# Kernel optimization log

Hardware: AMD Instinct MI355X
Metric: run time of the kernel (lower is better)

Reference implementation:

```python
import jax, jax.numpy as jnp
import numpy as np

N = 100000          # num_nodes
E = 1250000         # num_edges
H = 64              # node_hidden_size
T = 2               # num_rounds


def setup_inputs() -> dict:
    key = jax.random.key(0)
    ks = jax.random.split(key, 10)
    s = 0.1  # init scale for weights
    return {
        "x": jax.random.normal(ks[0], (N, H), dtype=jnp.float32),
        "edge_index": jax.random.randint(ks[1], (2, E), 0, N, dtype=jnp.int64),
        "edge_attr": jax.random.normal(ks[2], (E, 1), dtype=jnp.float32),
        # message layers: Linear(2H+1 -> H), one per round
        "msg_W": jax.random.normal(ks[3], (T, H, 2 * H + 1), dtype=jnp.float32) * s,
        "msg_b": jax.random.normal(ks[4], (T, H), dtype=jnp.float32) * s,
        # GRUCell params, gate order (r, z, n) as in torch
        "gru_Wih": jax.random.normal(ks[5], (T, 3 * H, H), dtype=jnp.float32) * s,
        "gru_bih": jax.random.normal(ks[6], (T, 3 * H), dtype=jnp.float32) * s,
        "gru_Whh": jax.random.normal(ks[7], (T, 3 * H, H), dtype=jnp.float32) * s,
        "gru_bhh": jax.random.normal(ks[8], (T, 3 * H), dtype=jnp.float32) * s,
    }


def _gru_cell(inp, h, Wih, bih, Whh, bhh):
    # torch.nn.GRUCell math, gate order r, z, n
    gi = inp @ Wih.T + bih   # [N, 3H]
    gh = h @ Whh.T + bhh     # [N, 3H]
    i_r, i_z, i_n = jnp.split(gi, 3, axis=1)
    h_r, h_z, h_n = jnp.split(gh, 3, axis=1)
    r = jax.nn.sigmoid(i_r + h_r)
    z = jax.nn.sigmoid(i_z + h_z)
    n = jnp.tanh(i_n + r * h_n)
    return (1.0 - z) * n + z * h


def reference(x, edge_index, edge_attr, msg_W, msg_b, gru_Wih, gru_bih, gru_Whh, gru_bhh):
    row, col = edge_index[0], edge_index[1]
    num_rounds = msg_W.shape[0]
    for t in range(num_rounds):
        src = x[row]    # [E, H]
        dest = x[col]   # [E, H]
        m_input = jnp.concatenate([dest, src, edge_attr], axis=1)  # [E, 2H+1]
        messages = m_input @ msg_W[t].T + msg_b[t]                 # [E, H]
        agg = jax.ops.segment_sum(messages, row, num_segments=x.shape[0])  # [N, H]
        x = _gru_cell(agg, x, gru_Wih[t], gru_bih[t], gru_Whh[t], gru_bhh[t])
    return x
```

## Files before the change

kernel.cpp:

```cpp
#include <hip/hip_runtime.h>
#include <hip/hip_bf16.h>
#include <hip/hip_fp16.h>

#define H 64
#define CAP 48

typedef __attribute__((ext_vector_type(8))) short short8;
typedef __attribute__((ext_vector_type(4))) float float4v;

__device__ __forceinline__ short f2bf_bits(float f) {
    union { __hip_bfloat16 b; short s; } u;
    u.b = __float2bfloat16(f);
    return u.s;
}
__device__ __forceinline__ float bf2f(unsigned short s) {
    union { unsigned int u; float f; } v;
    v.u = ((unsigned int)s) << 16;
    return v.f;
}
__device__ __forceinline__ void split8(const float* p, short8& hi, short8& lo) {
    float4v f0 = *(const float4v*)p;
    float4v f1 = *(const float4v*)(p + 4);
#pragma unroll
    for (int j = 0; j < 8; j++) {
        float f = (j < 4) ? f0[j] : f1[j - 4];
        short h = f2bf_bits(f);
        float fh = bf2f((unsigned short)h);
        hi[j] = h;
        lo[j] = f2bf_bits(f - fh);
    }
}
__device__ __forceinline__ void zero8(short8& hi, short8& lo) {
#pragma unroll
    for (int j = 0; j < 8; j++) { hi[j] = 0; lo[j] = 0; }
}

#define MFMA(a, b, c) __builtin_amdgcn_mfma_f32_16x16x32_bf16(a, b, c, 0, 0, 0)

__global__ __launch_bounds__(256) void count_prep(
    const int* __restrict__ row, int* __restrict__ deg, int* __restrict__ lpos,
    int E, int EB,
    const float* __restrict__ msg_W,
    const float* __restrict__ Wih, const float* __restrict__ Whh,
    short* __restrict__ msgfrag, short* __restrict__ grufrag, int T)
{
    if ((int)blockIdx.x < EB) {
        int e = blockIdx.x * 256 + threadIdx.x;
        if (e < E) lpos[e] = atomicAdd(&deg[row[e]], 1);
        return;
    }
    const int lane = threadIdx.x & 63;
    int unit = (blockIdx.x - EB) * 4 + (threadIdx.x >> 6);
    const int kq = (lane >> 4) * 8;
    if (unit < T * 16) {
        const int slot = unit & 15, t = unit >> 4;
        const int tile = slot >> 1, ks = slot & 1;
        const float* W = msg_W + (size_t)t * H * 129;
        const int wrow = (tile & 3) * 16 + (lane & 15);
        const int coff = (tile < 4) ? 0 : 64;
        short8 hi, lo;
        split8(W + (size_t)wrow * 129 + coff + ks * 32 + kq, hi, lo);
        short8* out = (short8*)(msgfrag + (size_t)t * 16384);
        out[slot * 64 + lane] = hi;
        out[16 * 64 + slot * 64 + lane] = lo;
    } else {
        unit -= T * 16;
        if (unit >= T * 48) return;
        const int slot = unit % 48, t = unit / 48;
        const int tile = slot >> 1, ks = slot & 1;
        const float* Wp = (tile < 12)
            ? (Wih + (size_t)t * 192 * H + ((size_t)(tile * 16 + (lane & 15))) * H)
            : (Whh + (size_t)t * 192 * H + ((size_t)((tile - 12) * 16 + (lane & 15))) * H);
        short8 hi, lo;
        split8(Wp + ks * 32 + kq, hi, lo);
        short8* out = (short8*)(grufrag + (size_t)t * 49152);
        out[slot * 64 + lane] = hi;
        out[48 * 64 + slot * 64 + lane] = lo;
    }
}

__global__ __launch_bounds__(256) void scatter_cast(
    const int* __restrict__ row, const int* __restrict__ col,
    const float* __restrict__ attr, const int* __restrict__ lpos,
    int2* __restrict__ edata, int E, int EB,
    const float* __restrict__ x_in, __half* __restrict__ xh, int NH8)
{
    if ((int)blockIdx.x < EB) {
        int e = blockIdx.x * 256 + threadIdx.x;
        if (e < E) {
            int p = lpos[e];
            if (p < CAP) {
                int2 v;
                v.x = col[e];
                v.y = __float_as_int(attr[e]);
                edata[(size_t)row[e] * CAP + p] = v;
            }
        }
    } else {
        int i = (blockIdx.x - EB) * 256 + threadIdx.x;
        if (i < NH8) {
            const float* p = x_in + (size_t)i * 8;
            float4v f0 = *(const float4v*)p;
            float4v f1 = *(const float4v*)(p + 4);
            short8 hv;
#pragma unroll
            for (int u = 0; u < 8; u++) {
                float f = (u < 4) ? f0[u] : f1[u - 4];
                hv[u] = __half_as_short(__float2half(f));
            }
            *(short8*)(xh + (size_t)i * 8) = hv;
        }
    }
}

__global__ __launch_bounds__(256) void aggregate(
    const int* __restrict__ deg, const int2* __restrict__ edata,
    const __half* __restrict__ xh,
    short* __restrict__ s_hi, short* __restrict__ s_lo,
    float2* __restrict__ asum2, int N)
{
    const int tid = threadIdx.x, lane = tid & 63, wv = tid >> 6;
    const int g = lane >> 3, cl = lane & 7;
    const int n = (blockIdx.x * 4 + wv) * 8 + g;
    int cnt = 0;
    if (n < N) { cnt = deg[n]; if (cnt > CAP) cnt = CAP; }
    const int2* ebase = edata + (size_t)n * CAP;
    float acc[8] = {0.f,0.f,0.f,0.f,0.f,0.f,0.f,0.f};
    float aacc = 0.f;
    for (int j = 0; j < cnt; j += 8) {
        int2 e[8];
#pragma unroll
        for (int u = 0; u < 8; u++) {
            int idx = j + u; if (idx > cnt - 1) idx = cnt - 1;
            e[u] = ebase[idx];
        }
        short8 h[8];
#pragma unroll
        for (int u = 0; u < 8; u++) {
            int c = e[u].x;
            c = (c < 0) ? 0 : (c >= N ? N - 1 : c);
            h[u] = *(const short8*)(xh + (size_t)c * H + cl * 8);
        }
#pragma unroll
        for (int u = 0; u < 8; u++) {
            const bool val = (j + u < cnt);
            const float w = val ? 1.f : 0.f;
            aacc += val ? __int_as_float(e[u].y) : 0.f;
#pragma unroll
            for (int k = 0; k < 8; k++)
                acc[k] = fmaf(w, __half2float(__ushort_as_half((unsigned short)h[u][k])), acc[k]);
        }
    }
    if (n < N) {
        short8 hi8, lo8;
#pragma unroll
        for (int u = 0; u < 8; u++) {
            float v = acc[u];
            short hbits = f2bf_bits(v);
            hi8[u] = hbits;
            lo8[u] = f2bf_bits(v - bf2f((unsigned short)hbits));
        }
        *(short8*)(s_hi + (size_t)n * H + cl * 8) = hi8;
        *(short8*)(s_lo + (size_t)n * H + cl * 8) = lo8;
        if (cl == 0) asum2[n] = make_float2(aacc, (float)cnt);
    }
}

#define SLD 68
__global__ __launch_bounds__(256) void fused_msg_gru(
    const short* __restrict__ s_hi, const short* __restrict__ s_lo,
    const float2* __restrict__ asum2,
    const float* xf,
    float* x, __half* __restrict__ xh,
    const short* __restrict__ mfrag, const short* __restrict__ gfrag,
    const float* __restrict__ Wt, const float* __restrict__ mb,
    const float* __restrict__ bih, const float* __restrict__ bhh,
    int N, int write_xh)
{
    __shared__ float scratch[4][16 * SLD];
    const int tid = threadIdx.x, lane = tid & 63, wv = tid >> 6;
    const int base = blockIdx.x * 64 + wv * 16;
    if (base >= N) return;
    const int arow = lane & 15;
    const int kq = (lane >> 4) * 8;
    const int colb = lane & 15;
    const int rq4 = (lane >> 4) * 4;
    const int m_a = base + arow;
    const bool mv = (m_a < N);
    const short8* mhi = (const short8*)mfrag;
    const short8* mlo = mhi + 16 * 64;
    const short8* ghi = (const short8*)gfrag;
    const short8* glo = ghi + 48 * 64;
    float* scr = scratch[wv];

    short8 sfh[2], sfl[2], xfh[2], xfl[2];
#pragma unroll
    for (int ks = 0; ks < 2; ks++) {
        if (mv) {
            sfh[ks] = *(const short8*)(s_hi + (size_t)m_a * H + ks * 32 + kq);
            sfl[ks] = *(const short8*)(s_lo + (size_t)m_a * H + ks * 32 + kq);
            split8(xf + (size_t)m_a * H + ks * 32 + kq, xfh[ks], xfl[ks]);
        } else { zero8(sfh[ks], sfl[ks]); zero8(xfh[ks], xfl[ks]); }
    }
    float2 da[4];
#pragma unroll
    for (int r = 0; r < 4; r++) {
        const int m = base + rq4 + r;
        da[r] = (m < N) ? asum2[m] : make_float2(0.f, 0.f);
    }

    float4v accd[4], accs[4];
#pragma unroll
    for (int ct = 0; ct < 4; ct++) {
        accd[ct] = (float4v){0.f, 0.f, 0.f, 0.f};
        accs[ct] = (float4v){0.f, 0.f, 0.f, 0.f};
    }
#pragma unroll
    for (int ks = 0; ks < 2; ks++) {
#pragma unroll
        for (int ct = 0; ct < 4; ct++) {
            short8 bh = mhi[(ct * 2 + ks) * 64 + lane];
            short8 bl = mlo[(ct * 2 + ks) * 64 + lane];
            accd[ct] = MFMA(sfh[ks], bh, accd[ct]);
            accd[ct] = MFMA(sfl[ks], bh, accd[ct]);
            accd[ct] = MFMA(sfh[ks], bl, accd[ct]);
            short8 ch = mhi[((4 + ct) * 2 + ks) * 64 + lane];
            short8 cl8 = mlo[((4 + ct) * 2 + ks) * 64 + lane];
            accs[ct] = MFMA(xfh[ks], ch, accs[ct]);
            accs[ct] = MFMA(xfl[ks], ch, accs[ct]);
            accs[ct] = MFMA(xfh[ks], cl8, accs[ct]);
        }
    }

#pragma unroll
    for (int ct = 0; ct < 4; ct++) {
        const int j = ct * 16 + colb;
        const float bj = mb[j];
        const float wa = Wt[(size_t)j * 129 + 128];
#pragma unroll
        for (int r = 0; r < 4; r++) {
            float v = accd[ct][r] + da[r].y * (accs[ct][r] + bj) + da[r].x * wa;
            scr[(rq4 + r) * SLD + j] = v;
        }
    }
    asm volatile("s_waitcnt lgkmcnt(0)" ::: "memory");
    short8 agh[2], agl[2];
#pragma unroll
    for (int ks = 0; ks < 2; ks++)
        split8(scr + arow * SLD + ks * 32 + kq, agh[ks], agl[ks]);

#pragma unroll
    for (int ct = 0; ct < 4; ct++) {
        float4v ai[3], ao[3];
#pragma unroll
        for (int g2 = 0; g2 < 3; g2++) {
            ai[g2] = (float4v){0.f, 0.f, 0.f, 0.f};
            ao[g2] = (float4v){0.f, 0.f, 0.f, 0.f};
        }
#pragma unroll
        for (int ks = 0; ks < 2; ks++) {
#pragma unroll
            for (int g2 = 0; g2 < 3; g2++) {
                short8 bh = ghi[((g2 * 4 + ct) * 2 + ks) * 64 + lane];
                short8 bl = glo[((g2 * 4 + ct) * 2 + ks) * 64 + lane];
                ai[g2] = MFMA(agh[ks], bh, ai[g2]);
                ai[g2] = MFMA(agl[ks], bh, ai[g2]);
                ai[g2] = MFMA(agh[ks], bl, ai[g2]);
                short8 hh = ghi[((12 + g2 * 4 + ct) * 2 + ks) * 64 + lane];
                short8 hl = glo[((12 + g2 * 4 + ct) * 2 + ks) * 64 + lane];
                ao[g2] = MFMA(xfh[ks], hh, ao[g2]);
                ao[g2] = MFMA(xfl[ks], hh, ao[g2]);
                ao[g2] = MFMA(xfh[ks], hl, ao[g2]);
            }
        }
        const int j = ct * 16 + colb;
        const float b_ir = bih[j], b_iz = bih[64 + j], b_in = bih[128 + j];
        const float b_hr = bhh[j], b_hz = bhh[64 + j], b_hn = bhh[128 + j];
#pragma unroll
        for (int r = 0; r < 4; r++) {
            const int m = base + rq4 + r;
            float ir = ai[0][r] + b_ir;
            float iz = ai[1][r] + b_iz;
            float in_ = ai[2][r] + b_in;
            float hr = ao[0][r] + b_hr;
            float hz = ao[1][r] + b_hz;
            float hn = ao[2][r] + b_hn;
            float rr = 1.f / (1.f + __expf(-(ir + hr)));
            float zz = 1.f / (1.f + __expf(-(iz + hz)));
            float e2 = __expf(2.f * (in_ + rr * hn));
            float nn = 1.f - 2.f / (e2 + 1.f);
            float hold = (m < N) ? xf[(size_t)m * H + j] : 0.f;
            scr[(rq4 + r) * SLD + j] = (1.f - zz) * nn + zz * hold;
        }
    }
    asm volatile("s_waitcnt lgkmcnt(0)" ::: "memory");

    if (mv) {
        float4v o[4];
#pragma unroll
        for (int q4 = 0; q4 < 4; q4++)
            o[q4] = *(const float4v*)(scr + arow * SLD + (lane >> 4) * 16 + q4 * 4);
        float4v* xp = (float4v*)(x + (size_t)m_a * H + (lane >> 4) * 16);
        xp[0] = o[0]; xp[1] = o[1]; xp[2] = o[2]; xp[3] = o[3];
        if (write_xh) {
            short8 hv0, hv1;
#pragma unroll
            for (int u = 0; u < 8; u++) {
                hv0[u] = __half_as_short(__float2half(o[u >> 2][u & 3]));
                hv1[u] = __half_as_short(__float2half(o[2 + (u >> 2)][u & 3]));
            }
            *(short8*)(xh + (size_t)m_a * H + (lane >> 4) * 16) = hv0;
            *(short8*)(xh + (size_t)m_a * H + (lane >> 4) * 16 + 8) = hv1;
        }
    }
}

extern "C" void kernel_launch(void* const* d_in, const int* in_sizes, int n_in,
                              void* d_out, int out_size, void* d_ws, size_t ws_size,
                              hipStream_t stream) {
    const float* x_in  = (const float*)d_in[0];
    const int*   ei    = (const int*)d_in[1];
    const float* attr  = (const float*)d_in[2];
    const float* msg_W = (const float*)d_in[3];
    const float* msg_b = (const float*)d_in[4];
    const float* Wih   = (const float*)d_in[5];
    const float* bih   = (const float*)d_in[6];
    const float* Whh   = (const float*)d_in[7];
    const float* bhh   = (const float*)d_in[8];

    const int N = in_sizes[0] / H;
    const int E = in_sizes[2];
    const int T = in_sizes[4] / H;
    const int* row = ei;
    const int* col = ei + E;

    float*  x       = (float*)d_out;
    short*  s_hi    = (short*)d_ws;
    short*  s_lo    = s_hi + (size_t)N * H;
    int*    lpos    = (int*)s_lo;
    __half* xh      = (__half*)(s_lo + (size_t)N * H);
    float2* asum2   = (float2*)(xh + (size_t)N * H);
    int*    deg     = (int*)(asum2 + N);
    int2*   edata   = (int2*)(deg + N);
    short*  msgfrag = (short*)(edata + (size_t)N * CAP);
    short*  grufrag = msgfrag + (size_t)T * 16384;

    const int eb  = (E + 255) / 256;
    const int nh8 = (N * H) / 8;
    const int cb  = (nh8 + 255) / 256;
    const int pb  = (T * 16 + T * 48 + 3) / 4;

    hipMemsetAsync(deg, 0, (size_t)N * sizeof(int), stream);

    count_prep<<<eb + pb, 256, 0, stream>>>(
        row, deg, lpos, E, eb, msg_W, Wih, Whh, msgfrag, grufrag, T);
    scatter_cast<<<eb + cb, 256, 0, stream>>>(
        row, col, attr, lpos, edata, E, eb, x_in, xh, nh8);

    const int nbq        = (N + 63) / 64;
    const int agg_blocks = (N + 31) / 32;

    for (int t = 0; t < T; t++) {
        aggregate<<<agg_blocks, 256, 0, stream>>>(
            deg, edata, xh, s_hi, s_lo, asum2, N);
        fused_msg_gru<<<nbq, 256, 0, stream>>>(
            s_hi, s_lo, asum2,
            (t == 0) ? x_in : x, x, xh,
            msgfrag + (size_t)t * 16384, grufrag + (size_t)t * 49152,
            msg_W + (size_t)t * H * (2 * H + 1), msg_b + (size_t)t * H,
            bih + (size_t)t * 3 * H, bhh + (size_t)t * 3 * H,
            N, (t + 1 < T) ? 1 : 0);
    }
}
```

Measured before the change: 343.6 us.

## Split edge counting across kernels, widen aggregate unroll, stage GRU weights in LDS

Edge counting is split into two halves: the first half's degree counting runs alongside weight prep and the fp16 cast of x, and the second half's counting runs alongside the scatter of the first half. This is meant to overlap atomic counting with scatter writes instead of running them in strict sequence. The aggregate kernel moves to 64-thread blocks and gathers 16 neighbours per iteration instead of 8, giving more loads in flight per wave. The fused GRU kernel now copies its 96KB of weight fragments into shared memory before computing, which costs LDS capacity and may reduce occupancy.

```diff
diff --git a/kernel.cpp b/kernel.cpp
--- a/kernel.cpp
+++ b/kernel.cpp
@@ -37,57 +37,79 @@
 
 #define MFMA(a, b, c) __builtin_amdgcn_mfma_f32_16x16x32_bf16(a, b, c, 0, 0, 0)
 
-__global__ __launch_bounds__(256) void count_prep(
+__global__ __launch_bounds__(256) void count_a(
     const int* __restrict__ row, int* __restrict__ deg, int* __restrict__ lpos,
-    int E, int EB,
+    int e1, int EB, int PB,
     const float* __restrict__ msg_W,
     const float* __restrict__ Wih, const float* __restrict__ Whh,
-    short* __restrict__ msgfrag, short* __restrict__ grufrag, int T)
-{
-    if ((int)blockIdx.x < EB) {
-        int e = blockIdx.x * 256 + threadIdx.x;
-        if (e < E) lpos[e] = atomicAdd(&deg[row[e]], 1);
-        return;
-    }
-    const int lane = threadIdx.x & 63;
-    int unit = (blockIdx.x - EB) * 4 + (threadIdx.x >> 6);
-    const int kq = (lane >> 4) * 8;
-    if (unit < T * 16) {
-        const int slot = unit & 15, t = unit >> 4;
-        const int tile = slot >> 1, ks = slot & 1;
-        const float* W = msg_W + (size_t)t * H * 129;
-        const int wrow = (tile & 3) * 16 + (lane & 15);
-        const int coff = (tile < 4) ? 0 : 64;
-        short8 hi, lo;
-        split8(W + (size_t)wrow * 129 + coff + ks * 32 + kq, hi, lo);
-        short8* out = (short8*)(msgfrag + (size_t)t * 16384);
-        out[slot * 64 + lane] = hi;
-        out[16 * 64 + slot * 64 + lane] = lo;
-    } else {
-        unit -= T * 16;
-        if (unit >= T * 48) return;
-        const int slot = unit % 48, t = unit / 48;
-        const int tile = slot >> 1, ks = slot & 1;
-        const float* Wp = (tile < 12)
-            ? (Wih + (size_t)t * 192 * H + ((size_t)(tile * 16 + (lane & 15))) * H)
-            : (Whh + (size_t)t * 192 * H + ((size_t)((tile - 12) * 16 + (lane & 15))) * H);
-        short8 hi, lo;
-        split8(Wp + ks * 32 + kq, hi, lo);
-        short8* out = (short8*)(grufrag + (size_t)t * 49152);
-        out[slot * 64 + lane] = hi;
-        out[48 * 64 + slot * 64 + lane] = lo;
-    }
-}
-
-__global__ __launch_bounds__(256) void scatter_cast(
-    const int* __restrict__ row, const int* __restrict__ col,
-    const float* __restrict__ attr, const int* __restrict__ lpos,
-    int2* __restrict__ edata, int E, int EB,
+    short* __restrict__ msgfrag, short* __restrict__ grufrag, int T,
     const float* __restrict__ x_in, __half* __restrict__ xh, int NH8)
 {
     if ((int)blockIdx.x < EB) {
         int e = blockIdx.x * 256 + threadIdx.x;
-        if (e < E) {
+        if (e < e1) lpos[e] = atomicAdd(&deg[row[e]], 1);
+        return;
+    }
+    int u = blockIdx.x - EB;
+    if (u < PB) {
+        const int lane = threadIdx.x & 63;
+        int unit = u * 4 + (threadIdx.x >> 6);
+        const int kq = (lane >> 4) * 8;
+        if (unit < T * 16) {
+            const int slot = unit & 15, t = unit >> 4;
+            const int tile = slot >> 1, ks = slot & 1;
+            const float* W = msg_W + (size_t)t * H * 129;
+            const int wrow = (tile & 3) * 16 + (lane & 15);
+            const int coff = (tile < 4) ? 0 : 64;
+            short8 hi, lo;
+            split8(W + (size_t)wrow * 129 + coff + ks * 32 + kq, hi, lo);
+            short8* out = (short8*)(msgfrag + (size_t)t * 16384);
+            out[slot * 64 + lane] = hi;
+            out[16 * 64 + slot * 64 + lane] = lo;
+        } else {
+            unit -= T * 16;
+            if (unit >= T * 48) return;
+            const int slot = unit % 48, t = unit / 48;
+            const int tile = slot >> 1, ks = slot & 1;
+            const float* Wp = (tile < 12)
+                ? (Wih + (size_t)t * 192 * H + ((size_t)(tile * 16 + (lane & 15))) * H)
+                : (Whh + (size_t)t * 192 * H + ((size_t)((tile - 12) * 16 + (lane & 15))) * H);
+            short8 hi, lo;
+            split8(Wp + ks * 32 + kq, hi, lo);
+            short8* out = (short8*)(grufrag + (size_t)t * 49152);
+            out[slot * 64 + lane] = hi;
+            out[48 * 64 + slot * 64 + lane] = lo;
+        }
+    } else {
+        int i = (u - PB) * 256 + threadIdx.x;
+        if (i < NH8) {
+            const float* p = x_in + (size_t)i * 8;
+            float4v f0 = *(const float4v*)p;
+            float4v f1 = *(const float4v*)(p + 4);
+            short8 hv;
+#pragma unroll
+            for (int v = 0; v < 8; v++) {
+                float f = (v < 4) ? f0[v] : f1[v - 4];
+                hv[v] = __half_as_short(__float2half(f));
+            }
+            *(short8*)(xh + (size_t)i * 8) = hv;
+        }
+    }
+}
+
+__global__ __launch_bounds__(256) void count_b(
+    const int* __restrict__ row, const int* __restrict__ col,
+    const float* __restrict__ attr,
+    int* __restrict__ deg, int* __restrict__ lpos,
+    int2* __restrict__ edata,
+    int c0, int E, int EBc, int s1)
+{
+    if ((int)blockIdx.x < EBc) {
+        int e = c0 + blockIdx.x * 256 + threadIdx.x;
+        if (e < E) lpos[e] = atomicAdd(&deg[row[e]], 1);
+    } else {
+        int e = (blockIdx.x - EBc) * 256 + threadIdx.x;
+        if (e < s1) {
             int p = lpos[e];
             if (p < CAP) {
                 int2 v;
@@ -96,53 +118,56 @@
                 edata[(size_t)row[e] * CAP + p] = v;
             }
         }
-    } else {
-        int i = (blockIdx.x - EB) * 256 + threadIdx.x;
-        if (i < NH8) {
-            const float* p = x_in + (size_t)i * 8;
-            float4v f0 = *(const float4v*)p;
-            float4v f1 = *(const float4v*)(p + 4);
-            short8 hv;
-#pragma unroll
-            for (int u = 0; u < 8; u++) {
-                float f = (u < 4) ? f0[u] : f1[u - 4];
-                hv[u] = __half_as_short(__float2half(f));
-            }
-            *(short8*)(xh + (size_t)i * 8) = hv;
-        }
-    }
-}
-
-__global__ __launch_bounds__(256) void aggregate(
+    }
+}
+
+__global__ __launch_bounds__(256) void scatter_b(
+    const int* __restrict__ row, const int* __restrict__ col,
+    const float* __restrict__ attr, const int* __restrict__ lpos,
+    int2* __restrict__ edata, int s0, int E)
+{
+    int e = s0 + blockIdx.x * 256 + threadIdx.x;
+    if (e < E) {
+        int p = lpos[e];
+        if (p < CAP) {
+            int2 v;
+            v.x = col[e];
+            v.y = __float_as_int(attr[e]);
+            edata[(size_t)row[e] * CAP + p] = v;
+        }
+    }
+}
+
+__global__ __launch_bounds__(64) void aggregate(
     const int* __restrict__ deg, const int2* __restrict__ edata,
     const __half* __restrict__ xh,
     short* __restrict__ s_hi, short* __restrict__ s_lo,
     float2* __restrict__ asum2, int N)
 {
-    const int tid = threadIdx.x, lane = tid & 63, wv = tid >> 6;
+    const int lane = threadIdx.x & 63;
     const int g = lane >> 3, cl = lane & 7;
-    const int n = (blockIdx.x * 4 + wv) * 8 + g;
+    const int n = blockIdx.x * 8 + g;
     int cnt = 0;
     if (n < N) { cnt = deg[n]; if (cnt > CAP) cnt = CAP; }
     const int2* ebase = edata + (size_t)n * CAP;
     float acc[8] = {0.f,0.f,0.f,0.f,0.f,0.f,0.f,0.f};
     float aacc = 0.f;
-    for (int j = 0; j < cnt; j += 8) {
-        int2 e[8];
-#pragma unroll
-        for (int u = 0; u < 8; u++) {
+    for (int j = 0; j < cnt; j += 16) {
+        int2 e[16];
+#pragma unroll
+        for (int u = 0; u < 16; u++) {
             int idx = j + u; if (idx > cnt - 1) idx = cnt - 1;
             e[u] = ebase[idx];
         }
-        short8 h[8];
-#pragma unroll
-        for (int u = 0; u < 8; u++) {
+        short8 h[16];
+#pragma unroll
+        for (int u = 0; u < 16; u++) {
             int c = e[u].x;
             c = (c < 0) ? 0 : (c >= N ? N - 1 : c);
             h[u] = *(const short8*)(xh + (size_t)c * H + cl * 8);
         }
 #pragma unroll
-        for (int u = 0; u < 8; u++) {
+        for (int u = 0; u < 16; u++) {
             const bool val = (j + u < cnt);
             const float w = val ? 1.f : 0.f;
             aacc += val ? __int_as_float(e[u].y) : 0.f;
@@ -177,8 +202,18 @@
     const float* __restrict__ bih, const float* __restrict__ bhh,
     int N, int write_xh)
 {
+    __shared__ short8 gls[6144];
     __shared__ float scratch[4][16 * SLD];
     const int tid = threadIdx.x, lane = tid & 63, wv = tid >> 6;
+
+    {
+        const short8* gsrc = (const short8*)gfrag;
+#pragma unroll
+        for (int i = 0; i < 24; i++)
+            gls[i * 256 + tid] = gsrc[i * 256 + tid];
+    }
+    __syncthreads();
+
     const int base = blockIdx.x * 64 + wv * 16;
     if (base >= N) return;
     const int arow = lane & 15;
@@ -189,8 +224,8 @@
     const bool mv = (m_a < N);
     const short8* mhi = (const short8*)mfrag;
     const short8* mlo = mhi + 16 * 64;
-    const short8* ghi = (const short8*)gfrag;
-    const short8* glo = ghi + 48 * 64;
+    const short8* ghi = gls;
+    const short8* glo = gls + 48 * 64;
     float* scr = scratch[wv];
 
     short8 sfh[2], sfl[2], xfh[2], xfl[2];
@@ -345,23 +380,28 @@
     short*  msgfrag = (short*)(edata + (size_t)N * CAP);
     short*  grufrag = msgfrag + (size_t)T * 16384;
 
-    const int eb  = (E + 255) / 256;
     const int nh8 = (N * H) / 8;
     const int cb  = (nh8 + 255) / 256;
     const int pb  = (T * 16 + T * 48 + 3) / 4;
 
+    const int EB0 = (E / 2) / 256;
+    const int E0  = EB0 * 256;
+    const int EB1 = (E - E0 + 255) / 256;
+
     hipMemsetAsync(deg, 0, (size_t)N * sizeof(int), stream);
 
-    count_prep<<<eb + pb, 256, 0, stream>>>(
-        row, deg, lpos, E, eb, msg_W, Wih, Whh, msgfrag, grufrag, T);
-    scatter_cast<<<eb + cb, 256, 0, stream>>>(
-        row, col, attr, lpos, edata, E, eb, x_in, xh, nh8);
-
+    count_a<<<EB0 + pb + cb, 256, 0, stream>>>(
+        row, deg, lpos, E0, EB0, pb, msg_W, Wih, Whh, msgfrag, grufrag, T,
+        x_in, xh, nh8);
+    count_b<<<EB1 + EB0, 256, 0, stream>>>(
+        row, col, attr, deg, lpos, edata, E0, E, EB1, E0);
+    scatter_b<<<EB1, 256, 0, stream>>>(row, col, attr, lpos, edata, E0, E);
+
+    const int agg_blocks = (N + 7) / 8;
     const int nbq        = (N + 63) / 64;
-    const int agg_blocks = (N + 31) / 32;
 
     for (int t = 0; t < T; t++) {
-        aggregate<<<agg_blocks, 256, 0, stream>>>(
+        aggregate<<<agg_blocks, 64, 0, stream>>>(
             deg, edata, xh, s_hi, s_lo, asum2, N);
         fused_msg_gru<<<nbq, 256, 0, stream>>>(
             s_hi, s_lo, asum2,
```

New measurement: 364.4 us. 1.06x slower.
